# Optimization experiments

Measured on AMD Instinct MI355X. Metric: run time of the kernel, lower is better.

## Reference

```python
import jax, jax.numpy as jnp
import numpy as np

B, C_IN, C_OUT = 16, 96, 192
N_IN, N_OUT, K = 16384, 4096, 16
SIGMA, MAX_ORD = 0.05, 2
M = 2 * MAX_ORD + 1  # basis size: 1 + cos/sin up to max_ord
BN_EPS = 1e-5


def _build_graph(rng):
    # random vertex layout; out vertices are a subset of in vertices
    vin = rng.standard_normal((N_IN, 2)).astype(np.float32)
    vout = vin[rng.choice(N_IN, N_OUT, replace=False)]
    idx = np.empty((N_OUT, K), np.int64)
    for s in range(0, N_OUT, 1024):  # chunked exact k-NN
        d = ((vout[s:s + 1024, None, :] - vin[None, :, :]) ** 2).sum(-1)
        idx[s:s + 1024] = np.argpartition(d, K, axis=1)[:, :K]
    rel = vin[idx] - vout[:, None, :]            # [N_out, K, 2]
    r2 = (rel ** 2).sum(-1)
    theta = np.arctan2(rel[..., 1], rel[..., 0])
    gauss = np.exp(-r2 / (2.0 * SIGMA ** 2))
    harm = [np.ones_like(theta)]
    for m in range(1, MAX_ORD + 1):
        harm += [np.cos(m * theta), np.sin(m * theta)]
    basis = (gauss[..., None] * np.stack(harm, -1)).astype(np.float32)  # [N_out, K, M]
    return idx, basis


def setup_inputs() -> dict:
    rng = np.random.default_rng(0)
    idx, basis = _build_graph(rng)
    key = jax.random.key(0)
    k0, k1, k2 = jax.random.split(key, 3)
    return {
        "x": jax.random.normal(k0, (B, C_IN, N_IN), jnp.float32),
        "idx": jnp.asarray(idx),
        "basis": jnp.asarray(basis),
        "conv_w": jax.random.normal(k1, (C_OUT, C_IN, M), jnp.float32) * 0.02,
        "conv_b": jnp.zeros((C_OUT,), jnp.float32),
        "pool_w": jax.random.normal(k2, (C_OUT, C_IN), jnp.float32) * 0.02,
        "pool_b": jnp.zeros((C_OUT,), jnp.float32),
        "gamma": jnp.ones((C_OUT,), jnp.float32),
        "beta": jnp.zeros((C_OUT,), jnp.float32),
    }


def reference(x, idx, basis, conv_w, conv_b, pool_w, pool_b, gamma, beta):
    # irregular k-NN gather: [B, C_in, N_out, K]
    neigh = x[:, :, idx]
    # identity path: AvgPool over k neighbors + 1x1 conv
    pooled = neigh.mean(axis=-1)                                   # [B, C_in, N_out]
    identity = jnp.einsum('oc,bcn->bon', pool_w, pooled) + pool_b[:, None]
    # ConvV2: project neighbors onto gaussian-harmonic basis, contract with weights
    feat = jnp.einsum('bcnk,nkm->bcnm', neigh, basis)              # [B, C_in, N_out, M]
    out = jnp.einsum('ocm,bcnm->bon', conv_w, feat) + conv_b[:, None]
    # BatchNorm1d (training-mode batch stats over B and N)
    mean = out.mean(axis=(0, 2), keepdims=True)
    var = out.var(axis=(0, 2), keepdims=True)
    out = (out - mean) * jax.lax.rsqrt(var + BN_EPS) * gamma[:, None] + beta[:, None]
    return out + identity
```

## Files before the change

### kernel.cpp

```cpp
#include <hip/hip_runtime.h>

typedef __attribute__((ext_vector_type(8))) short s16x8;
typedef __attribute__((ext_vector_type(4))) float f32x4;

constexpr int cB = 16, cCIN = 96, cCOUT = 192, cNIN = 16384, cNOUT = 4096, cK = 16;
constexpr float cEPS = 1e-5f;

constexpr size_t OFF_XT     = 0;
constexpr size_t OFF_CONVB  = 0;
constexpr size_t OFF_IDENTB = 25165824;
constexpr size_t OFF_FEATA  = 50331648;
constexpr size_t OFF_WB     = 125829120;
constexpr size_t OFF_SS     = 126050304;

__device__ inline unsigned bf16_rne(float f) {
    unsigned u = __builtin_bit_cast(unsigned, f);
    return (u + 0x7fffu + ((u >> 16) & 1u)) >> 16;
}
__device__ inline float bf16_f(unsigned short h) {
    unsigned u = ((unsigned)h) << 16;
    return __builtin_bit_cast(float, u);
}

__launch_bounds__(256)
__global__ void k_tr(const float* __restrict__ x, unsigned* __restrict__ xto) {
    __shared__ float s[96 * 133];
    const int b = blockIdx.y, j0 = blockIdx.x * 128, t = threadIdx.x;
    const float* xb = x + (size_t)b * 96 * 16384 + j0;
    for (int q = t; q < 3072; q += 256) {
        int c = q >> 5, j4 = (q & 31) * 4;
        float4 v = *(const float4*)(xb + (size_t)c * 16384 + j4);
        s[c * 133 + j4 + 0] = v.x;
        s[c * 133 + j4 + 1] = v.y;
        s[c * 133 + j4 + 2] = v.z;
        s[c * 133 + j4 + 3] = v.w;
    }
    __syncthreads();
    for (int q = t; q < 6144; q += 256) {
        int cp = q % 48, jj = q / 48;
        float f0 = s[(2 * cp) * 133 + jj];
        float f1 = s[(2 * cp + 1) * 133 + jj];
        unsigned pr = bf16_rne(f0) | (bf16_rne(f1) << 16);
        xto[(size_t)(b * 16384 + j0 + jj) * 48 + cp] = pr;
    }
}

__global__ void k_pack(const float* __restrict__ cw, const float* __restrict__ pw,
                       unsigned short* __restrict__ wB) {
    int e = blockIdx.x * 256 + threadIdx.x;
    if (e >= 110592) return;
    int r = e & 7, l = (e >> 3) & 63;
    int ts = e >> 9;
    int s = ts % 18, ot = ts / 18;
    int o = ot * 16 + (l & 15);
    int ko = s * 32 + ((l >> 4) << 3) + r;
    float v;
    if (ko < 480) { int m = ko / 96, c = ko % 96; v = cw[(o * 96 + c) * 5 + m]; }
    else          { int c = ko - 480;             v = pw[o * 96 + c]; }
    wB[e] = (unsigned short)bf16_rne(v);
}

__launch_bounds__(192)
__global__ void k_feat(const unsigned short* __restrict__ xt,
                       const int* __restrict__ idx,
                       const float* __restrict__ basis,
                       unsigned short* __restrict__ featA) {
    __shared__ float s_bas[16 * 97];
    __shared__ int s_idx[256];
    const int t = threadIdx.x, b = blockIdx.y, n0 = blockIdx.x * 16;

    for (int i = t; i < 256; i += 192)
        s_idx[i] = idx[n0 * 16 + i];
    for (int i = t; i < 16 * 96; i += 192) {
        int nl = i / 96, km = i % 96, k = km / 6, m = km % 6;
        float v = (m < 5) ? basis[((size_t)(n0 + nl) * 16 + k) * 5 + m] : 0.0625f;
        s_bas[nl * 97 + km] = v;
    }
    __syncthreads();

    const int c8 = t >> 4, nl = t & 15;
    float fm[6][8];
#pragma unroll
    for (int m = 0; m < 6; ++m)
#pragma unroll
        for (int j = 0; j < 8; ++j) fm[m][j] = 0.f;

    const size_t xbase = (size_t)b * 16384;
#pragma unroll 4
    for (int k = 0; k < 16; ++k) {
        int j = s_idx[nl * 16 + k];
        s16x8 v = *(const s16x8*)(xt + (xbase + j) * 96 + c8 * 8);
        float gf[8];
#pragma unroll
        for (int q = 0; q < 8; ++q) gf[q] = bf16_f((unsigned short)v[q]);
#pragma unroll
        for (int m = 0; m < 6; ++m) {
            float bv = s_bas[nl * 97 + k * 6 + m];
#pragma unroll
            for (int q = 0; q < 8; ++q) fm[m][q] = fmaf(gf[q], bv, fm[m][q]);
        }
    }

    const int tile = b * 256 + blockIdx.x;
    const int fl = nl + ((c8 & 3) << 4);
#pragma unroll
    for (int m = 0; m < 6; ++m) {
        int s = 3 * m + (c8 >> 2);
        uint4 o;
        o.x = bf16_rne(fm[m][0]) | (bf16_rne(fm[m][1]) << 16);
        o.y = bf16_rne(fm[m][2]) | (bf16_rne(fm[m][3]) << 16);
        o.z = bf16_rne(fm[m][4]) | (bf16_rne(fm[m][5]) << 16);
        o.w = bf16_rne(fm[m][6]) | (bf16_rne(fm[m][7]) << 16);
        *(uint4*)(featA + ((size_t)(tile * 18 + s) * 64 + fl) * 8) = o;
    }
}

__launch_bounds__(256)
__global__ void k_gemm(const unsigned short* __restrict__ featA,
                       const unsigned short* __restrict__ wB,
                       unsigned short* __restrict__ convb,
                       unsigned short* __restrict__ identb) {
    __shared__ __align__(16) unsigned short s_c[192 * 72];
    const int t = threadIdx.x;
    const int w = t >> 6, lane = t & 63;
    const int wr = w & 1, wc = w >> 1;
    const int bid = blockIdx.x;
    const int tile0 = bid * 4 + wr * 2;
    const s16x8* A  = (const s16x8*)featA;
    const s16x8* Bw = (const s16x8*)wB;

    f32x4 accC[2][6], accI[2][6];
    const f32x4 z = {0.f, 0.f, 0.f, 0.f};
#pragma unroll
    for (int rt = 0; rt < 2; ++rt)
#pragma unroll
        for (int j = 0; j < 6; ++j) { accC[rt][j] = z; accI[rt][j] = z; }

    for (int s = 0; s < 15; ++s) {
        s16x8 a0 = A[(size_t)(tile0 * 18 + s) * 64 + lane];
        s16x8 a1 = A[(size_t)((tile0 + 1) * 18 + s) * 64 + lane];
#pragma unroll
        for (int j = 0; j < 6; ++j) {
            s16x8 bf = Bw[(size_t)((wc * 6 + j) * 18 + s) * 64 + lane];
            accC[0][j] = __builtin_amdgcn_mfma_f32_16x16x32_bf16(a0, bf, accC[0][j], 0, 0, 0);
            accC[1][j] = __builtin_amdgcn_mfma_f32_16x16x32_bf16(a1, bf, accC[1][j], 0, 0, 0);
        }
    }
#pragma unroll
    for (int s = 15; s < 18; ++s) {
        s16x8 a0 = A[(size_t)(tile0 * 18 + s) * 64 + lane];
        s16x8 a1 = A[(size_t)((tile0 + 1) * 18 + s) * 64 + lane];
#pragma unroll
        for (int j = 0; j < 6; ++j) {
            s16x8 bf = Bw[(size_t)((wc * 6 + j) * 18 + s) * 64 + lane];
            accI[0][j] = __builtin_amdgcn_mfma_f32_16x16x32_bf16(a0, bf, accI[0][j], 0, 0, 0);
            accI[1][j] = __builtin_amdgcn_mfma_f32_16x16x32_bf16(a1, bf, accI[1][j], 0, 0, 0);
        }
    }

    const int col_l = lane & 15, rg = (lane >> 4) * 4;
    const int b  = (bid * 64) >> 12;
    const int n0 = (bid * 64) & 4095;

#pragma unroll
    for (int rt = 0; rt < 2; ++rt) {
        int lr = (wr * 2 + rt) * 16 + rg;
#pragma unroll
        for (int j = 0; j < 6; ++j) {
            int o = (wc * 6 + j) * 16 + col_l;
#pragma unroll
            for (int r = 0; r < 4; ++r)
                s_c[o * 72 + lr + r] = (unsigned short)bf16_rne(accC[rt][j][r]);
        }
    }
    __syncthreads();
    for (int u = t; u < 1536; u += 256) {
        int o = u >> 3, part = u & 7;
        uint4 v = *(const uint4*)(&s_c[o * 72 + part * 8]);
        *(uint4*)(convb + ((size_t)(b * 192 + o)) * 4096 + n0 + part * 8) = v;
    }
    __syncthreads();
#pragma unroll
    for (int rt = 0; rt < 2; ++rt) {
        int lr = (wr * 2 + rt) * 16 + rg;
#pragma unroll
        for (int j = 0; j < 6; ++j) {
            int o = (wc * 6 + j) * 16 + col_l;
#pragma unroll
            for (int r = 0; r < 4; ++r)
                s_c[o * 72 + lr + r] = (unsigned short)bf16_rne(accI[rt][j][r]);
        }
    }
    __syncthreads();
    for (int u = t; u < 1536; u += 256) {
        int o = u >> 3, part = u & 7;
        uint4 v = *(const uint4*)(&s_c[o * 72 + part * 8]);
        *(uint4*)(identb + ((size_t)(b * 192 + o)) * 4096 + n0 + part * 8) = v;
    }
}

__launch_bounds__(256)
__global__ void k_stats(const unsigned short* __restrict__ convb,
                        const float* __restrict__ gamma,
                        const float* __restrict__ beta,
                        const float* __restrict__ pool_b,
                        float* __restrict__ ss) {
    int o = blockIdx.x, t = threadIdx.x;
    float s1 = 0.f, s2 = 0.f;
    for (int b = 0; b < cB; ++b) {
        const uint4* p = (const uint4*)(convb + ((size_t)b * cCOUT + o) * cNOUT);
        for (int q = t; q < 512; q += 256) {
            uint4 v = p[q];
            const unsigned short* h = (const unsigned short*)&v;
#pragma unroll
            for (int j = 0; j < 8; ++j) {
                float f = bf16_f(h[j]);
                s1 += f;
                s2 = fmaf(f, f, s2);
            }
        }
    }
#pragma unroll
    for (int off = 32; off; off >>= 1) {
        s1 += __shfl_down(s1, off);
        s2 += __shfl_down(s2, off);
    }
    __shared__ float w1[4], w2[4];
    int lane = t & 63, wid = t >> 6;
    if (lane == 0) { w1[wid] = s1; w2[wid] = s2; }
    __syncthreads();
    if (t == 0) {
        float S1 = w1[0] + w1[1] + w1[2] + w1[3];
        float S2 = w2[0] + w2[1] + w2[2] + w2[3];
        float inv  = 1.0f / (cB * cNOUT);
        float mean = S1 * inv;
        float var  = S2 * inv - mean * mean;
        float scale = gamma[o] * rsqrtf(var + cEPS);
        ss[o]         = scale;
        ss[cCOUT + o] = beta[o] - mean * scale + pool_b[o];
    }
}

__launch_bounds__(256)
__global__ void k_final(const unsigned short* __restrict__ convb,
                        const unsigned short* __restrict__ identb,
                        const float* __restrict__ ss,
                        float* __restrict__ out) {
    size_t i = ((size_t)blockIdx.x * 256 + threadIdx.x) * 8;
    int o = (int)((i >> 12) % cCOUT);
    uint4 cv = *(const uint4*)(convb + i);
    uint4 dv = *(const uint4*)(identb + i);
    const unsigned short* ch = (const unsigned short*)&cv;
    const unsigned short* dh = (const unsigned short*)&dv;
    float sc = ss[o], sh = ss[cCOUT + o];
    float r[8];
#pragma unroll
    for (int j = 0; j < 8; ++j)
        r[j] = fmaf(bf16_f(ch[j]), sc, sh + bf16_f(dh[j]));
    *(float4*)(out + i)     = *(float4*)&r[0];
    *(float4*)(out + i + 4) = *(float4*)&r[4];
}

extern "C" void kernel_launch(void* const* d_in, const int* in_sizes, int n_in,
                              void* d_out, int out_size, void* d_ws, size_t ws_size,
                              hipStream_t stream) {
    const float* x      = (const float*)d_in[0];
    const int*   idx    = (const int*)d_in[1];
    const float* basis  = (const float*)d_in[2];
    const float* conv_w = (const float*)d_in[3];
    const float* pool_w = (const float*)d_in[5];
    const float* pool_b = (const float*)d_in[6];
    const float* gamma  = (const float*)d_in[7];
    const float* beta   = (const float*)d_in[8];
    float* out = (float*)d_out;

    char* wsb = (char*)d_ws;
    unsigned short* xt     = (unsigned short*)(wsb + OFF_XT);
    unsigned short* convb  = (unsigned short*)(wsb + OFF_CONVB);
    unsigned short* identb = (unsigned short*)(wsb + OFF_IDENTB);
    unsigned short* featA  = (unsigned short*)(wsb + OFF_FEATA);
    unsigned short* wB     = (unsigned short*)(wsb + OFF_WB);
    float*          ss     = (float*)(wsb + OFF_SS);

    k_tr   <<<dim3(cNIN / 128, cB), 256, 0, stream>>>(x, (unsigned*)xt);
    k_pack <<<(110592 + 255) / 256, 256, 0, stream>>>(conv_w, pool_w, wB);
    k_feat <<<dim3(cNOUT / 16, cB), 192, 0, stream>>>(xt, idx, basis, featA);
    k_gemm <<<(cB * cNOUT) / 64, 256, 0, stream>>>(featA, wB, convb, identb);
    k_stats<<<cCOUT, 256, 0, stream>>>(convb, gamma, beta, pool_b, ss);
    k_final<<<(size_t)cB * cCOUT * cNOUT / 2048, 256, 0, stream>>>(convb, identb, ss, out);
}
```

Before: 150.2 us.

## Fuse BatchNorm partial sums into GEMM epilogue and shrink stats kernel

The GEMM epilogue now reduces per-channel sum and sum-of-squares over its tile rows with cross-lane shuffles and writes the partials to workspace. The separate stats kernel only sums 2048 partials per channel instead of re-reading the whole bf16 conv output (about 25 MB). Statistics are taken from the fp32 accumulators rather than the bf16-rounded values, which slightly changes numerics, and the GEMM epilogue gets a little extra work.

Result: faster. 145.5 us (-3.1%).

```diff
diff --git a/kernel.cpp b/kernel.cpp
--- a/kernel.cpp
+++ b/kernel.cpp
@@ -3,7 +3,7 @@
 typedef __attribute__((ext_vector_type(8))) short s16x8;
 typedef __attribute__((ext_vector_type(4))) float f32x4;
 
-constexpr int cB = 16, cCIN = 96, cCOUT = 192, cNIN = 16384, cNOUT = 4096, cK = 16;
+constexpr int cB = 16, cCIN = 96, cCOUT = 192, cNIN = 16384, cNOUT = 4096;
 constexpr float cEPS = 1e-5f;
 
 constexpr size_t OFF_XT     = 0;
@@ -12,6 +12,8 @@
 constexpr size_t OFF_FEATA  = 50331648;
 constexpr size_t OFF_WB     = 125829120;
 constexpr size_t OFF_SS     = 126050304;
+constexpr size_t OFF_S1     = 126051840;
+constexpr size_t OFF_S2     = 127624704;
 
 __device__ inline unsigned bf16_rne(float f) {
     unsigned u = __builtin_bit_cast(unsigned, f);
@@ -119,7 +121,9 @@
 __global__ void k_gemm(const unsigned short* __restrict__ featA,
                        const unsigned short* __restrict__ wB,
                        unsigned short* __restrict__ convb,
-                       unsigned short* __restrict__ identb) {
+                       unsigned short* __restrict__ identb,
+                       float* __restrict__ s1g,
+                       float* __restrict__ s2g) {
     __shared__ __align__(16) unsigned short s_c[192 * 72];
     const int t = threadIdx.x;
     const int w = t >> 6, lane = t & 63;
@@ -163,6 +167,26 @@
     const int n0 = (bid * 64) & 4095;
 
 #pragma unroll
+    for (int j = 0; j < 6; ++j) {
+        float s1 = 0.f, s2 = 0.f;
+#pragma unroll
+        for (int rt = 0; rt < 2; ++rt)
+#pragma unroll
+            for (int r = 0; r < 4; ++r) {
+                float v = accC[rt][j][r];
+                s1 += v;
+                s2 = fmaf(v, v, s2);
+            }
+        s1 += __shfl_xor(s1, 16); s2 += __shfl_xor(s2, 16);
+        s1 += __shfl_xor(s1, 32); s2 += __shfl_xor(s2, 32);
+        if (lane < 16) {
+            int o = (wc * 6 + j) * 16 + lane;
+            s1g[(size_t)o * 2048 + bid * 2 + wr] = s1;
+            s2g[(size_t)o * 2048 + bid * 2 + wr] = s2;
+        }
+    }
+
+#pragma unroll
     for (int rt = 0; rt < 2; ++rt) {
         int lr = (wr * 2 + rt) * 16 + rg;
 #pragma unroll
@@ -200,25 +224,14 @@
 }
 
 __launch_bounds__(256)
-__global__ void k_stats(const unsigned short* __restrict__ convb,
-                        const float* __restrict__ gamma,
-                        const float* __restrict__ beta,
-                        const float* __restrict__ pool_b,
-                        float* __restrict__ ss) {
+__global__ void k_ss(const float* __restrict__ s1g, const float* __restrict__ s2g,
+                     const float* __restrict__ gamma, const float* __restrict__ beta,
+                     const float* __restrict__ pool_b, float* __restrict__ ss) {
     int o = blockIdx.x, t = threadIdx.x;
     float s1 = 0.f, s2 = 0.f;
-    for (int b = 0; b < cB; ++b) {
-        const uint4* p = (const uint4*)(convb + ((size_t)b * cCOUT + o) * cNOUT);
-        for (int q = t; q < 512; q += 256) {
-            uint4 v = p[q];
-            const unsigned short* h = (const unsigned short*)&v;
-#pragma unroll
-            for (int j = 0; j < 8; ++j) {
-                float f = bf16_f(h[j]);
-                s1 += f;
-                s2 = fmaf(f, f, s2);
-            }
-        }
+    for (int i = t; i < 2048; i += 256) {
+        s1 += s1g[(size_t)o * 2048 + i];
+        s2 += s2g[(size_t)o * 2048 + i];
     }
 #pragma unroll
     for (int off = 32; off; off >>= 1) {
@@ -281,11 +294,13 @@
     unsigned short* featA  = (unsigned short*)(wsb + OFF_FEATA);
     unsigned short* wB     = (unsigned short*)(wsb + OFF_WB);
     float*          ss     = (float*)(wsb + OFF_SS);
+    float*          s1g    = (float*)(wsb + OFF_S1);
+    float*          s2g    = (float*)(wsb + OFF_S2);
 
     k_tr   <<<dim3(cNIN / 128, cB), 256, 0, stream>>>(x, (unsigned*)xt);
     k_pack <<<(110592 + 255) / 256, 256, 0, stream>>>(conv_w, pool_w, wB);
     k_feat <<<dim3(cNOUT / 16, cB), 192, 0, stream>>>(xt, idx, basis, featA);
-    k_gemm <<<(cB * cNOUT) / 64, 256, 0, stream>>>(featA, wB, convb, identb);
-    k_stats<<<cCOUT, 256, 0, stream>>>(convb, gamma, beta, pool_b, ss);
+    k_gemm <<<(cB * cNOUT) / 64, 256, 0, stream>>>(featA, wB, convb, identb, s1g, s2g);
+    k_ss   <<<cCOUT, 256, 0, stream>>>(s1g, s2g, gamma, beta, pool_b, ss);
     k_final<<<(size_t)cB * cCOUT * cNOUT / 2048, 256, 0, stream>>>(convb, identb, ss, out);
 }
```
